# Optimization experiments

Hardware: AMD Instinct MI355X
Metric: run time of the kernel (lower is better)

The kernel has to match this reference:

```python
import jax, jax.numpy as jnp
import numpy as np

B, N, H, L, K, R = 1024, 64, 128, 4, 16, 20
CUTOFF = 5.0
GAMMA = 10.0   # RBF width
N_TYPES = 10

def _rn(k, shape, scale):
    return jax.random.normal(k, shape, jnp.float32) * scale

def setup_inputs():
    key = jax.random.key(0)
    ks = jax.random.split(key, 16)
    z = lambda *s: jnp.zeros(s, jnp.float32)
    return {
        "positions": _rn(ks[0], (B, N, 3), 2.0),
        "atomic_numbers": jax.random.randint(ks[1], (B, N), 0, N_TYPES),
        "atom_embed": _rn(ks[2], (N_TYPES, H // 4), 0.1),
        "pos_W": _rn(ks[3], (3, 3 * H // 4), 0.5),
        "pos_b": z(3 * H // 4),
        "msg_W": _rn(ks[4], (L, 2 * H + R, H), (2 * H + R) ** -0.5),
        "msg_b": z(L, H),
        "upd_W": _rn(ks[5], (L, H, H), H ** -0.5),
        "upd_b": z(L, H),
        "gself_W": _rn(ks[6], (L, H, H), H ** -0.5),
        "gmean_W": _rn(ks[7], (L, H, H), H ** -0.5),
        "g_b": z(L, H),
        "fus_W": _rn(ks[8], (L, 2 * H, H), (2 * H) ** -0.5),
        "fus_b": z(L, H),
        "ln_g": jnp.ones((L, H), jnp.float32),
        "ln_b": z(L, H),
        "cb_W1": _rn(ks[9], (L, H, 4 * H), H ** -0.5),
        "cb_b1": z(L, 4 * H),
        "cb_W2": _rn(ks[10], (L, 4 * H, H), (4 * H) ** -0.5),
        "cb_b2": z(L, H),
        "fo_W1": _rn(ks[11], (H, H), H ** -0.5),
        "fo_b1": z(H),
        "fo_W2": _rn(ks[12], (H, 3), H ** -0.5),
        "fo_b2": z(3),
    }

def _ln(x, g, b):
    m = x.mean(-1, keepdims=True)
    v = ((x - m) ** 2).mean(-1, keepdims=True)
    return (x - m) * jax.lax.rsqrt(v + 1e-5) * g + b

def reference(positions, atomic_numbers, atom_embed, pos_W, pos_b, msg_W, msg_b,
              upd_W, upd_b, gself_W, gmean_W, g_b, fus_W, fus_b, ln_g, ln_b,
              cb_W1, cb_b1, cb_W2, cb_b2, fo_W1, fo_b1, fo_W2, fo_b2):
    silu = jax.nn.silu
    Bb, Nn, _ = positions.shape
    # embeddings: atom type (H/4) || position (3H/4)
    h = jnp.concatenate([atom_embed[atomic_numbers], positions @ pos_W + pos_b], -1)  # [B,N,H]
    # kNN graph from positions (static across layers since positions are fixed)
    diff = positions[:, :, None, :] - positions[:, None, :, :]
    d2 = jnp.sum(diff * diff, -1) + jnp.eye(Nn, dtype=positions.dtype) * 1e9  # exclude self
    neg_d2, idx = jax.lax.top_k(-d2, K)                       # [B,N,K]
    d = jnp.sqrt(jnp.maximum(-neg_d2, 1e-12))
    centers = jnp.linspace(0.0, CUTOFF, R).astype(positions.dtype)
    rbf = jnp.exp(-GAMMA * (d[..., None] - centers) ** 2)     # [B,N,K,R]
    env = (0.5 * (jnp.cos(jnp.pi * d / CUTOFF) + 1.0) * (d < CUTOFF))[..., None]  # cosine cutoff
    idx_flat = idx.reshape(Bb, Nn * K)
    for i in range(msg_W.shape[0]):
        # local MPNN: gather neighbors, message MLP on [h_i, h_j, rbf], envelope, sum
        h_j = jnp.take_along_axis(h, idx_flat[:, :, None], axis=1).reshape(Bb, Nn, K, -1)
        h_i = jnp.broadcast_to(h[:, :, None, :], h_j.shape)
        m = silu(jnp.concatenate([h_i, h_j, rbf], -1) @ msg_W[i] + msg_b[i]) * env
        local = h + silu(m.sum(2) @ upd_W[i] + upd_b[i])
        # Clifford mean-field: self transform + global-mean transform
        glob = silu(h @ gself_W[i] + h.mean(1, keepdims=True) @ gmean_W[i] + g_b[i])
        # fusion (dropout is identity at inference)
        fused = silu(jnp.concatenate([local, glob], -1) @ fus_W[i] + fus_b[i])
        # Clifford block: pre-LN residual MLP
        x = _ln(fused, ln_g[i], ln_b[i])
        h = fused + silu(x @ cb_W1[i] + cb_b1[i]) @ cb_W2[i] + cb_b2[i]
    return silu(h @ fo_W1 + fo_b1) @ fo_W2 + fo_b2  # [B,N,3] forces
```

## Files before the change

kernel.cpp:

```cpp
#include <hip/hip_runtime.h>

typedef unsigned short ushort_t;
typedef unsigned int uint_t;
typedef unsigned long long ull_t;
typedef __attribute__((ext_vector_type(8))) short short8;
typedef __attribute__((ext_vector_type(4))) float f32x4;

#define B_ 1024
#define N_ 64
#define H_ 128
#define NT 256

#define IMG_WI 0
#define IMG_WJ 16384
#define IMG_UW 32768
#define IMG_GS 49152
#define IMG_FT 65536
#define IMG_FB 81920
#define IMG_C1 98304
#define IMG_C2 163840
#define IMG_GMT 229376
#define IMG_RW 245760
#define IMG_L 249856
#define IMG_FO 999424
#define WS_WEIGHTS (2u*1024u*1024u)
#define KNN_STRIDE 12288u

__device__ __forceinline__ ushort_t f2bf(float f) {
    uint_t u = __float_as_uint(f);
    return (ushort_t)((u + 0x7fffu + ((u >> 16) & 1u)) >> 16);
}
__device__ __forceinline__ float bf2f(ushort_t u) {
    union { uint_t i; float f; } v; v.i = ((uint_t)u) << 16; return v.f;
}
__device__ __forceinline__ float siluf(float x) { return x / (1.0f + __expf(-x)); }

__device__ __forceinline__ int sidx(int m, int k) {
    return m * H_ + (((k >> 3) ^ (m & 7)) << 3) + (k & 7);
}
__device__ __forceinline__ int fragoff(int m, int ch) {
    return m * H_ + ((ch ^ (m & 7)) << 3);
}

extern "C" __global__ __launch_bounds__(256)
void convert_weights(const float* __restrict__ msg_W, const float* __restrict__ upd_W,
                     const float* __restrict__ gself_W, const float* __restrict__ fus_W,
                     const float* __restrict__ cb_W1, const float* __restrict__ cb_W2,
                     const float* __restrict__ gmean_W, const float* __restrict__ fo_W1,
                     ushort_t* __restrict__ wimg)
{
    const int g = blockIdx.x;
    if (g >= 244) {
        int st = g - 244;
        ushort_t* dst = wimg + IMG_FO + st * 4096;
        for (int e = 0; e < 16; ++e) {
            int q = threadIdx.x * 16 + e;
            int n = q >> 7, k = q & 127;
            dst[q] = f2bf(fo_W1[(size_t)k * 128 + st * 32 + n]);
        }
        return;
    }
    const int l = g / 61, r = g - l * 61;
    ushort_t* base = wimg + l * IMG_L;
    if (r == 60) {
        const float* W = msg_W + l * 35328 + 256 * 128;
        ushort_t* dst = base + IMG_RW;
        for (int e = 0; e < 16; ++e) {
            int q = threadIdx.x * 16 + e;
            int sub = q >> 10, n = (q >> 5) & 31, k = q & 31;
            dst[q] = f2bf(k < 20 ? W[(size_t)k * 128 + sub * 32 + n] : 0.0f);
        }
        return;
    }
    const float* W; int ld = 128, k0 = 0, c0, off, st;
    if      (r < 4)  { W = msg_W + l * 35328;            st = r;      off = IMG_WI;  c0 = st * 32; }
    else if (r < 8)  { W = msg_W + l * 35328;  k0 = 128; st = r - 4;  off = IMG_WJ;  c0 = st * 32; }
    else if (r < 12) { W = upd_W + l * 16384;            st = r - 8;  off = IMG_UW;  c0 = st * 32; }
    else if (r < 16) { W = gself_W + l * 16384;          st = r - 12; off = IMG_GS;  c0 = st * 32; }
    else if (r < 20) { W = fus_W + l * 32768;            st = r - 16; off = IMG_FT;  c0 = st * 32; }
    else if (r < 24) { W = fus_W + l * 32768;  k0 = 128; st = r - 20; off = IMG_FB;  c0 = st * 32; }
    else if (r < 40) { W = cb_W1 + l * 65536;  ld = 512; st = r - 24; off = IMG_C1;  c0 = st * 32; }
    else if (r < 56) { int j = (r - 40) >> 2; W = cb_W2 + l * 65536; k0 = j * 128;
                       st = r - 40; off = IMG_C2; c0 = ((r - 40) & 3) * 32; }
    else             { W = gmean_W + l * 16384;          st = r - 56; off = IMG_GMT; c0 = st * 32; }
    ushort_t* dst = base + off + st * 4096;
    for (int e = 0; e < 16; ++e) {
        int q = threadIdx.x * 16 + e;
        int n = q >> 7, k = q & 127;
        dst[q] = f2bf(W[(size_t)(k0 + k) * ld + c0 + n]);
    }
}

extern "C" __global__ __launch_bounds__(64)
void knn_kernel(const float* __restrict__ positions, char* __restrict__ ws)
{
    const int b = blockIdx.x, lane = threadIdx.x;
    float px = positions[b * 192 + lane * 3 + 0];
    float py = positions[b * 192 + lane * 3 + 1];
    float pz = positions[b * 192 + lane * 3 + 2];
    float* kd = (float*)(ws + WS_WEIGHTS + (size_t)b * KNN_STRIDE);
    float* ke = kd + 1024;
    ushort_t* ki = (ushort_t*)(ke + 1024);
    for (int n = 0; n < 64; ++n) {
        float dx = __fsub_rn(__shfl(px, n), px);
        float dy = __fsub_rn(__shfl(py, n), py);
        float dz = __fsub_rn(__shfl(pz, n), pz);
        float d2 = __fadd_rn(__fadd_rn(__fmul_rn(dx, dx), __fmul_rn(dy, dy)), __fmul_rn(dz, dz));
        if (lane == n) d2 = 1e30f;
        float sd = 0.f; int si = 0;
        for (int k = 0; k < 16; ++k) {
            float dmin = d2;
            #pragma unroll
            for (int o = 1; o < 64; o <<= 1) dmin = fminf(dmin, __shfl_xor(dmin, o));
            ull_t mask = __ballot(d2 == dmin);
            int widx = __ffsll(mask) - 1;
            if (lane == widx) d2 = 1e30f;
            if (lane == k) { si = widx; sd = dmin; }
        }
        if (lane < 16) {
            float dd = sqrtf(fmaxf(sd, 1e-12f));
            kd[n * 16 + lane] = dd;
            ke[n * 16 + lane] = (dd < 5.0f) ? 0.5f * (__cosf(0.62831853071795864769f * dd) + 1.0f) : 0.0f;
            ki[n * 16 + lane] = (ushort_t)si;
        }
    }
}

struct __align__(16) Smem {
    ushort_t T1[N_ * H_];
    ushort_t T2[N_ * H_];
    ushort_t T3[N_ * H_];
    float d[1024];
    float env[1024];
    ushort_t idx[1024];
    char u[2048];
};

__device__ __forceinline__ f32x4 gemm_s(const short8 a[4], const ushort_t* __restrict__ img,
                                        int s, int l15, int quad)
{
    const ushort_t* base = img + ((s >> 1) << 12) + ((((s & 1) << 4) + l15) << 7) + quad * 8;
    short8 b0 = *(const short8*)(base);
    short8 b1 = *(const short8*)(base + 32);
    short8 b2 = *(const short8*)(base + 64);
    short8 b3 = *(const short8*)(base + 96);
    f32x4 c = {0.f, 0.f, 0.f, 0.f};
    c = __builtin_amdgcn_mfma_f32_16x16x32_bf16(a[0], b0, c, 0, 0, 0);
    c = __builtin_amdgcn_mfma_f32_16x16x32_bf16(a[1], b1, c, 0, 0, 0);
    c = __builtin_amdgcn_mfma_f32_16x16x32_bf16(a[2], b2, c, 0, 0, 0);
    c = __builtin_amdgcn_mfma_f32_16x16x32_bf16(a[3], b3, c, 0, 0, 0);
    return c;
}
__device__ __forceinline__ f32x4 gemm_s_acc(const short8 a[4], const ushort_t* __restrict__ img,
                                            int s, int l15, int quad, f32x4 c)
{
    const ushort_t* base = img + ((s >> 1) << 12) + ((((s & 1) << 4) + l15) << 7) + quad * 8;
    short8 b0 = *(const short8*)(base);
    short8 b1 = *(const short8*)(base + 32);
    short8 b2 = *(const short8*)(base + 64);
    short8 b3 = *(const short8*)(base + 96);
    c = __builtin_amdgcn_mfma_f32_16x16x32_bf16(a[0], b0, c, 0, 0, 0);
    c = __builtin_amdgcn_mfma_f32_16x16x32_bf16(a[1], b1, c, 0, 0, 0);
    c = __builtin_amdgcn_mfma_f32_16x16x32_bf16(a[2], b2, c, 0, 0, 0);
    c = __builtin_amdgcn_mfma_f32_16x16x32_bf16(a[3], b3, c, 0, 0, 0);
    return c;
}
__device__ __forceinline__ void loadA(const ushort_t* __restrict__ X, int mrow, int quad, short8 a[4]) {
    #pragma unroll
    for (int kc = 0; kc < 4; ++kc) a[kc] = *(const short8*)&X[fragoff(mrow, kc * 4 + quad)];
}

extern "C" __global__ __launch_bounds__(NT, 2)
void md17_fused_kernel(
    const float* __restrict__ positions, const int* __restrict__ atomic_numbers,
    const float* __restrict__ atom_embed, const float* __restrict__ pos_W,
    const float* __restrict__ pos_b,
    const float* __restrict__ msg_b, const float* __restrict__ upd_b,
    const float* __restrict__ g_b, const float* __restrict__ fus_b,
    const float* __restrict__ ln_g, const float* __restrict__ ln_b,
    const float* __restrict__ cb_b1, const float* __restrict__ cb_b2,
    const float* __restrict__ fo_b1,
    const float* __restrict__ fo_W2, const float* __restrict__ fo_b2,
    char* __restrict__ ws, float* __restrict__ out)
{
    __shared__ Smem sm;
    const int b = blockIdx.x;
    const int tid = threadIdx.x;
    const int wave = tid >> 6, lane = tid & 63;
    const int quad = lane >> 4, l15 = lane & 15;
    const int mrow = wave * 16 + l15;
    const int rbase = wave * 16 + quad * 4;

    const ushort_t* wimg = (const ushort_t*)ws;
    float* spos = (float*)sm.u;
    ushort_t* part = (ushort_t*)sm.u;
    float* hmean = (float*)(sm.u + 1024);
    float* gvec  = (float*)(sm.u + 1536);

    float hreg[8][4];

    {
        const char* kb = ws + WS_WEIGHTS + (size_t)b * KNN_STRIDE;
        const float* kd = (const float*)kb;
        const float* ke = (const float*)(kb + 4096);
        const uint_t* ki = (const uint_t*)(kb + 8192);
        for (int t = tid; t < 1024; t += NT) { sm.d[t] = kd[t]; sm.env[t] = ke[t]; }
        for (int t = tid; t < 512; t += NT) ((uint_t*)sm.idx)[t] = ki[t];
        if (tid < 192) spos[tid] = positions[b * 192 + tid];
    }
    __syncthreads();
    {
        int an[4];
        #pragma unroll
        for (int r = 0; r < 4; ++r) an[r] = atomic_numbers[b * N_ + rbase + r];
        #pragma unroll
        for (int s = 0; s < 8; ++s) {
            int col = s * 16 + l15;
            #pragma unroll
            for (int r = 0; r < 4; ++r) {
                float v;
                if (s < 2) {
                    v = atom_embed[an[r] * 32 + col];
                } else {
                    int j = col - 32;
                    v = pos_b[j];
                    #pragma unroll
                    for (int c = 0; c < 3; ++c)
                        v = fmaf(spos[(rbase + r) * 3 + c], pos_W[c * 96 + j], v);
                }
                hreg[s][r] = v;
                sm.T3[sidx(rbase + r, col)] = f2bf(v);
            }
        }
    }
    __syncthreads();

    #pragma unroll 1
    for (int l = 0; l < 4; ++l) {
        const ushort_t* wl = wimg + l * IMG_L;
        const float* mb  = msg_b + l * H_;
        const float* ub  = upd_b + l * H_;
        const float* gb  = g_b + l * H_;
        const float* fb  = fus_b + l * H_;
        const float* lg  = ln_g + l * H_;
        const float* lb  = ln_b + l * H_;
        const float* c1b = cb_b1 + l * 4 * H_;
        const float* c2b = cb_b2 + l * H_;

        #pragma unroll
        for (int s = 0; s < 8; ++s) {
            int col = s * 16 + l15;
            float p = hreg[s][0] + hreg[s][1] + hreg[s][2] + hreg[s][3];
            p += __shfl_xor(p, 16);
            p += __shfl_xor(p, 32);
            if (quad == 0) part[wave * 128 + col] = f2bf(p);
        }
        __syncthreads();
        if (tid < H_)
            hmean[tid] = (bf2f(part[tid]) + bf2f(part[128 + tid])
                        + bf2f(part[256 + tid]) + bf2f(part[384 + tid])) * (1.0f / 64.0f);
        __syncthreads();

        if (tid < H_) {
            float s = gb[tid];
            const ushort_t* wrow = wl + IMG_GMT + tid * 128;
            for (int c = 0; c < 128; c += 8) {
                short8 w = *(const short8*)(wrow + c);
                #pragma unroll
                for (int i = 0; i < 8; ++i) s = fmaf(hmean[c + i], bf2f((ushort_t)w[i]), s);
            }
            gvec[tid] = s;
        }
        {
            short8 a_h[4]; loadA(sm.T3, mrow, quad, a_h);
            #pragma unroll
            for (int s = 0; s < 8; ++s) {
                f32x4 c = gemm_s(a_h, wl + IMG_WI, s, l15, quad);
                int col = s * 16 + l15; float bv = mb[col];
                #pragma unroll
                for (int r = 0; r < 4; ++r)
                    sm.T1[sidx(rbase + r, col)] = f2bf(c[r] + bv);
            }
            #pragma unroll
            for (int s = 0; s < 8; ++s) {
                f32x4 c = gemm_s(a_h, wl + IMG_WJ, s, l15, quad);
                int col = s * 16 + l15;
                #pragma unroll
                for (int r = 0; r < 4; ++r)
                    sm.T2[sidx(rbase + r, col)] = f2bf(c[r]);
            }
        }
        __syncthreads();

        {
            float ccv[8];
            #pragma unroll
            for (int j = 0; j < 8; ++j)
                ccv[j] = (float)((double)(quad * 8 + j) * (5.0 / 19.0));
            #pragma unroll 1
            for (int g = 0; g < 16; ++g) {
                int n = wave * 16 + g;
                int jv[4]; float ev[4];
                #pragma unroll
                for (int r = 0; r < 4; ++r) {
                    int k = quad * 4 + r;
                    jv[r] = sm.idx[n * 16 + k];
                    ev[r] = sm.env[n * 16 + k];
                }
                float ddm = sm.d[n * 16 + l15];
                short8 arb;
                #pragma unroll
                for (int j = 0; j < 8; ++j) {
                    float t2 = ddm - ccv[j];
                    float rv = __expf(-10.0f * t2 * t2);
                    arb[j] = (short)((quad * 8 + j) < 20 ? f2bf(rv) : (ushort_t)0);
                }
                #pragma unroll
                for (int s = 0; s < 8; ++s) {
                    int col = s * 16 + l15;
                    const ushort_t* rbase_p = wl + IMG_RW + ((s >> 1) << 10)
                                            + ((((s & 1) << 4) + l15) << 5) + quad * 8;
                    short8 brw = *(const short8*)rbase_p;
                    f32x4 c = {0.f, 0.f, 0.f, 0.f};
                    c = __builtin_amdgcn_mfma_f32_16x16x32_bf16(arb, brw, c, 0, 0, 0);
                    float ai = bf2f(sm.T1[sidx(n, col)]);
                    float acc = 0.f;
                    #pragma unroll
                    for (int r = 0; r < 4; ++r) {
                        float gm = bf2f(sm.T2[sidx(jv[r], col)]);
                        acc = fmaf(siluf(ai + gm + c[r]), ev[r], acc);
                    }
                    acc += __shfl_xor(acc, 16);
                    acc += __shfl_xor(acc, 32);
                    if (quad == 0) sm.T1[sidx(n, col)] = f2bf(acc);
                }
            }
        }
        __syncthreads();


        {
            short8 a_m[4]; loadA(sm.T1, mrow, quad, a_m);
            #pragma unroll
            for (int s = 0; s < 8; ++s) {
                f32x4 c = gemm_s(a_m, wl + IMG_UW, s, l15, quad);
                int col = s * 16 + l15; float bv = ub[col];
                #pragma unroll
                for (int r = 0; r < 4; ++r)
                    sm.T2[sidx(rbase + r, col)] = f2bf(hreg[s][r] + siluf(c[r] + bv));
            }
            short8 a_h[4]; loadA(sm.T3, mrow, quad, a_h);
            #pragma unroll
            for (int s = 0; s < 8; ++s) {
                f32x4 c = gemm_s(a_h, wl + IMG_GS, s, l15, quad);
                int col = s * 16 + l15; float gv = gvec[col];
                #pragma unroll
                for (int r = 0; r < 4; ++r)
                    sm.T1[sidx(rbase + r, col)] = f2bf(siluf(c[r] + gv));
            }
        }

        float sr[4] = {0.f, 0.f, 0.f, 0.f}, qr[4] = {0.f, 0.f, 0.f, 0.f};
        {
            short8 a_t[4];
            loadA(sm.T2, mrow, quad, a_t);
            #pragma unroll
            for (int s = 0; s < 8; ++s) {
                f32x4 c = gemm_s(a_t, wl + IMG_FT, s, l15, quad);
                #pragma unroll
                for (int r = 0; r < 4; ++r) hreg[s][r] = c[r];
            }
            loadA(sm.T1, mrow, quad, a_t);
            #pragma unroll
            for (int s = 0; s < 8; ++s) {
                f32x4 c = gemm_s(a_t, wl + IMG_FB, s, l15, quad);
                int col = s * 16 + l15; float bv = fb[col];
                #pragma unroll
                for (int r = 0; r < 4; ++r) {
                    float v = siluf(hreg[s][r] + c[r] + bv);
                    hreg[s][r] = v;
                    sr[r] += v; qr[r] += v * v;
                }
            }
            #pragma unroll
            for (int o = 1; o < 16; o <<= 1) {
                #pragma unroll
                for (int r = 0; r < 4; ++r) {
                    sr[r] += __shfl_xor(sr[r], o);
                    qr[r] += __shfl_xor(qr[r], o);
                }
            }
        }

        #pragma unroll
        for (int r = 0; r < 4; ++r) {
            float mu = sr[r] * (1.0f / 128.0f);
            float var = qr[r] * (1.0f / 128.0f) - mu * mu;
            float rs = rsqrtf(var + 1e-5f);
            int row = rbase + r;
            #pragma unroll
            for (int s = 0; s < 8; ++s) {
                int col = s * 16 + l15;
                sm.T1[sidx(row, col)] = f2bf((hreg[s][r] - mu) * rs * lg[col] + lb[col]);
            }
        }

        {
            f32x4 acc2[8];
            #pragma unroll
            for (int s = 0; s < 8; ++s) {
                int col = s * 16 + l15; float bv = c2b[col];
                #pragma unroll
                for (int r = 0; r < 4; ++r) acc2[s][r] = hreg[s][r] + bv;
            }
            #pragma unroll 1
            for (int j = 0; j < 4; ++j) {
                short8 a_x[4]; loadA(sm.T1, mrow, quad, a_x);
                #pragma unroll
                for (int s = 0; s < 8; ++s) {
                    f32x4 c = gemm_s(a_x, wl + IMG_C1 + j * 16384, s, l15, quad);
                    int col = s * 16 + l15; float bv = c1b[j * H_ + col];
                    #pragma unroll
                    for (int r = 0; r < 4; ++r)
                        sm.T2[sidx(rbase + r, col)] = f2bf(siluf(c[r] + bv));
                }
                short8 a_t[4]; loadA(sm.T2, mrow, quad, a_t);
                #pragma unroll
                for (int s = 0; s < 8; ++s)
                    acc2[s] = gemm_s_acc(a_t, wl + IMG_C2 + j * 16384, s, l15, quad, acc2[s]);
            }
            #pragma unroll
            for (int s = 0; s < 8; ++s) {
                #pragma unroll
                for (int r = 0; r < 4; ++r) {
                    float v = acc2[s][r];
                    hreg[s][r] = v;
                    sm.T3[sidx(rbase + r, s * 16 + l15)] = f2bf(v);
                }
            }
        }
    }

    {
        short8 a_f[4]; loadA(sm.T3, mrow, quad, a_f);
        #pragma unroll
        for (int s = 0; s < 8; ++s) {
            f32x4 c = gemm_s(a_f, wimg + IMG_FO, s, l15, quad);
            int col = s * 16 + l15; float bv = fo_b1[col];
            #pragma unroll
            for (int r = 0; r < 4; ++r)
                sm.T2[sidx(rbase + r, col)] = f2bf(siluf(c[r] + bv));
        }
    }
    __syncthreads();
    if (tid < 192) {
        int n = tid / 3, j = tid - n * 3;
        float s = fo_b2[j];
        #pragma unroll 1
        for (int ch = 0; ch < 16; ++ch) {
            short8 v = *(const short8*)&sm.T2[fragoff(n, ch)];
            #pragma unroll
            for (int i = 0; i < 8; ++i)
                s = fmaf(bf2f((ushort_t)v[i]), fo_W2[(ch * 8 + i) * 3 + j], s);
        }
        out[b * 192 + tid] = s;
    }
}

extern "C" void kernel_launch(void* const* d_in, const int* in_sizes, int n_in,
                              void* d_out, int out_size, void* d_ws, size_t ws_size,
                              hipStream_t stream) {
    (void)in_sizes; (void)n_in; (void)out_size; (void)ws_size;
    convert_weights<<<248, 256, 0, stream>>>(
        (const float*)d_in[5], (const float*)d_in[7], (const float*)d_in[9],
        (const float*)d_in[12], (const float*)d_in[16], (const float*)d_in[18],
        (const float*)d_in[10], (const float*)d_in[20], (ushort_t*)d_ws);
    knn_kernel<<<B_, 64, 0, stream>>>((const float*)d_in[0], (char*)d_ws);
    md17_fused_kernel<<<B_, NT, 0, stream>>>(
        (const float*)d_in[0], (const int*)d_in[1],
        (const float*)d_in[2], (const float*)d_in[3], (const float*)d_in[4],
        (const float*)d_in[6], (const float*)d_in[8],
        (const float*)d_in[11], (const float*)d_in[13],
        (const float*)d_in[14], (const float*)d_in[15],
        (const float*)d_in[17], (const float*)d_in[19],
        (const float*)d_in[21],
        (const float*)d_in[22], (const float*)d_in[23],
        (char*)d_ws, (float*)d_out);
}
```

Baseline: 1.434 ms.

## Fuse kNN into main kernel, tile weight conversion via LDS, hoist RBF weights

```diff
diff --git a/kernel.cpp b/kernel.cpp
--- a/kernel.cpp
+++ b/kernel.cpp
@@ -23,12 +23,9 @@
 #define IMG_RW 245760
 #define IMG_L 249856
 #define IMG_FO 999424
-#define WS_WEIGHTS (2u*1024u*1024u)
-#define KNN_STRIDE 12288u
 
 __device__ __forceinline__ ushort_t f2bf(float f) {
-    uint_t u = __float_as_uint(f);
-    return (ushort_t)((u + 0x7fffu + ((u >> 16) & 1u)) >> 16);
+    return __builtin_bit_cast(ushort_t, (__bf16)f);
 }
 __device__ __forceinline__ float bf2f(ushort_t u) {
     union { uint_t i; float f; } v; v.i = ((uint_t)u) << 16; return v.f;
@@ -49,80 +46,55 @@
                      const float* __restrict__ gmean_W, const float* __restrict__ fo_W1,
                      ushort_t* __restrict__ wimg)
 {
+    __shared__ ushort_t tile[128][34];
     const int g = blockIdx.x;
+    const int tid = threadIdx.x;
+    const float* W; int ld = 128, k0 = 0, c0; ushort_t* dst;
     if (g >= 244) {
         int st = g - 244;
-        ushort_t* dst = wimg + IMG_FO + st * 4096;
-        for (int e = 0; e < 16; ++e) {
-            int q = threadIdx.x * 16 + e;
-            int n = q >> 7, k = q & 127;
-            dst[q] = f2bf(fo_W1[(size_t)k * 128 + st * 32 + n]);
-        }
-        return;
-    }
-    const int l = g / 61, r = g - l * 61;
-    ushort_t* base = wimg + l * IMG_L;
-    if (r == 60) {
-        const float* W = msg_W + l * 35328 + 256 * 128;
-        ushort_t* dst = base + IMG_RW;
-        for (int e = 0; e < 16; ++e) {
-            int q = threadIdx.x * 16 + e;
-            int sub = q >> 10, n = (q >> 5) & 31, k = q & 31;
-            dst[q] = f2bf(k < 20 ? W[(size_t)k * 128 + sub * 32 + n] : 0.0f);
-        }
-        return;
-    }
-    const float* W; int ld = 128, k0 = 0, c0, off, st;
-    if      (r < 4)  { W = msg_W + l * 35328;            st = r;      off = IMG_WI;  c0 = st * 32; }
-    else if (r < 8)  { W = msg_W + l * 35328;  k0 = 128; st = r - 4;  off = IMG_WJ;  c0 = st * 32; }
-    else if (r < 12) { W = upd_W + l * 16384;            st = r - 8;  off = IMG_UW;  c0 = st * 32; }
-    else if (r < 16) { W = gself_W + l * 16384;          st = r - 12; off = IMG_GS;  c0 = st * 32; }
-    else if (r < 20) { W = fus_W + l * 32768;            st = r - 16; off = IMG_FT;  c0 = st * 32; }
-    else if (r < 24) { W = fus_W + l * 32768;  k0 = 128; st = r - 20; off = IMG_FB;  c0 = st * 32; }
-    else if (r < 40) { W = cb_W1 + l * 65536;  ld = 512; st = r - 24; off = IMG_C1;  c0 = st * 32; }
-    else if (r < 56) { int j = (r - 40) >> 2; W = cb_W2 + l * 65536; k0 = j * 128;
-                       st = r - 40; off = IMG_C2; c0 = ((r - 40) & 3) * 32; }
-    else             { W = gmean_W + l * 16384;          st = r - 56; off = IMG_GMT; c0 = st * 32; }
-    ushort_t* dst = base + off + st * 4096;
-    for (int e = 0; e < 16; ++e) {
-        int q = threadIdx.x * 16 + e;
-        int n = q >> 7, k = q & 127;
-        dst[q] = f2bf(W[(size_t)(k0 + k) * ld + c0 + n]);
-    }
-}
-
-extern "C" __global__ __launch_bounds__(64)
-void knn_kernel(const float* __restrict__ positions, char* __restrict__ ws)
-{
-    const int b = blockIdx.x, lane = threadIdx.x;
-    float px = positions[b * 192 + lane * 3 + 0];
-    float py = positions[b * 192 + lane * 3 + 1];
-    float pz = positions[b * 192 + lane * 3 + 2];
-    float* kd = (float*)(ws + WS_WEIGHTS + (size_t)b * KNN_STRIDE);
-    float* ke = kd + 1024;
-    ushort_t* ki = (ushort_t*)(ke + 1024);
-    for (int n = 0; n < 64; ++n) {
-        float dx = __fsub_rn(__shfl(px, n), px);
-        float dy = __fsub_rn(__shfl(py, n), py);
-        float dz = __fsub_rn(__shfl(pz, n), pz);
-        float d2 = __fadd_rn(__fadd_rn(__fmul_rn(dx, dx), __fmul_rn(dy, dy)), __fmul_rn(dz, dz));
-        if (lane == n) d2 = 1e30f;
-        float sd = 0.f; int si = 0;
-        for (int k = 0; k < 16; ++k) {
-            float dmin = d2;
-            #pragma unroll
-            for (int o = 1; o < 64; o <<= 1) dmin = fminf(dmin, __shfl_xor(dmin, o));
-            ull_t mask = __ballot(d2 == dmin);
-            int widx = __ffsll(mask) - 1;
-            if (lane == widx) d2 = 1e30f;
-            if (lane == k) { si = widx; sd = dmin; }
-        }
-        if (lane < 16) {
-            float dd = sqrtf(fmaxf(sd, 1e-12f));
-            kd[n * 16 + lane] = dd;
-            ke[n * 16 + lane] = (dd < 5.0f) ? 0.5f * (__cosf(0.62831853071795864769f * dd) + 1.0f) : 0.0f;
-            ki[n * 16 + lane] = (ushort_t)si;
-        }
+        W = fo_W1; c0 = st * 32; dst = wimg + IMG_FO + st * 4096;
+    } else {
+        const int l = g / 61, r = g - l * 61;
+        ushort_t* base = wimg + l * IMG_L;
+        if (r == 60) {
+            const float* Wr = msg_W + l * 35328 + 256 * 128;
+            ushort_t* drw = base + IMG_RW;
+            for (int e = 0; e < 16; ++e) {
+                int q = threadIdx.x * 16 + e;
+                int sub = q >> 10, n = (q >> 5) & 31, k = q & 31;
+                drw[q] = f2bf(k < 20 ? Wr[(size_t)k * 128 + sub * 32 + n] : 0.0f);
+            }
+            return;
+        }
+        int off, st;
+        if      (r < 4)  { W = msg_W + l * 35328;            st = r;      off = IMG_WI;  c0 = st * 32; }
+        else if (r < 8)  { W = msg_W + l * 35328;  k0 = 128; st = r - 4;  off = IMG_WJ;  c0 = st * 32; }
+        else if (r < 12) { W = upd_W + l * 16384;            st = r - 8;  off = IMG_UW;  c0 = st * 32; }
+        else if (r < 16) { W = gself_W + l * 16384;          st = r - 12; off = IMG_GS;  c0 = st * 32; }
+        else if (r < 20) { W = fus_W + l * 32768;            st = r - 16; off = IMG_FT;  c0 = st * 32; }
+        else if (r < 24) { W = fus_W + l * 32768;  k0 = 128; st = r - 20; off = IMG_FB;  c0 = st * 32; }
+        else if (r < 40) { W = cb_W1 + l * 65536;  ld = 512; st = r - 24; off = IMG_C1;  c0 = st * 32; }
+        else if (r < 56) { int j = (r - 40) >> 2; W = cb_W2 + l * 65536; k0 = j * 128;
+                           st = r - 40; off = IMG_C2; c0 = ((r - 40) & 3) * 32; }
+        else             { W = gmean_W + l * 16384;          st = r - 56; off = IMG_GMT; c0 = st * 32; }
+        dst = base + off + st * 4096;
+    }
+    const int kr = tid >> 5, n = tid & 31;
+    #pragma unroll
+    for (int p = 0; p < 16; ++p) {
+        int k = p * 8 + kr;
+        tile[k][n] = f2bf(W[(size_t)(k0 + k) * ld + c0 + n]);
+    }
+    __syncthreads();
+    {
+        int n2 = tid >> 3, kk = (tid & 7) << 4;
+        short8 v0, v1;
+        #pragma unroll
+        for (int e = 0; e < 8; ++e) v0[e] = (short)tile[kk + e][n2];
+        #pragma unroll
+        for (int e = 0; e < 8; ++e) v1[e] = (short)tile[kk + 8 + e][n2];
+        *(short8*)(dst + n2 * 128 + kk) = v0;
+        *(short8*)(dst + n2 * 128 + kk + 8) = v1;
     }
 }
 
@@ -200,13 +172,35 @@
     float hreg[8][4];
 
     {
-        const char* kb = ws + WS_WEIGHTS + (size_t)b * KNN_STRIDE;
-        const float* kd = (const float*)kb;
-        const float* ke = (const float*)(kb + 4096);
-        const uint_t* ki = (const uint_t*)(kb + 8192);
-        for (int t = tid; t < 1024; t += NT) { sm.d[t] = kd[t]; sm.env[t] = ke[t]; }
-        for (int t = tid; t < 512; t += NT) ((uint_t*)sm.idx)[t] = ki[t];
+        float px = positions[b * 192 + lane * 3 + 0];
+        float py = positions[b * 192 + lane * 3 + 1];
+        float pz = positions[b * 192 + lane * 3 + 2];
         if (tid < 192) spos[tid] = positions[b * 192 + tid];
+        #pragma unroll 1
+        for (int g = 0; g < 16; ++g) {
+            int n = wave * 16 + g;
+            float dx = __fsub_rn(__shfl(px, n), px);
+            float dy = __fsub_rn(__shfl(py, n), py);
+            float dz = __fsub_rn(__shfl(pz, n), pz);
+            float d2 = __fadd_rn(__fadd_rn(__fmul_rn(dx, dx), __fmul_rn(dy, dy)), __fmul_rn(dz, dz));
+            if (lane == n) d2 = 1e30f;
+            float sd = 0.f; int si = 0;
+            for (int k = 0; k < 16; ++k) {
+                float dmin = d2;
+                #pragma unroll
+                for (int o = 1; o < 64; o <<= 1) dmin = fminf(dmin, __shfl_xor(dmin, o));
+                ull_t mask = __ballot(d2 == dmin);
+                int widx = __ffsll(mask) - 1;
+                if (lane == widx) d2 = 1e30f;
+                if (lane == k) { si = widx; sd = dmin; }
+            }
+            if (lane < 16) {
+                float dd = sqrtf(fmaxf(sd, 1e-12f));
+                sm.d[n * 16 + lane] = dd;
+                sm.env[n * 16 + lane] = (dd < 5.0f) ? 0.5f * (__cosf(0.62831853071795864769f * dd) + 1.0f) : 0.0f;
+                sm.idx[n * 16 + lane] = (ushort_t)si;
+            }
+        }
     }
     __syncthreads();
     {
@@ -234,6 +228,14 @@
         }
     }
     __syncthreads();
+    #pragma unroll
+    for (int s = 0; s < 8; ++s) {
+        int col = s * 16 + l15;
+        float p = hreg[s][0] + hreg[s][1] + hreg[s][2] + hreg[s][3];
+        p += __shfl_xor(p, 16);
+        p += __shfl_xor(p, 32);
+        if (quad == 0) part[wave * 128 + col] = f2bf(p);
+    }
 
     #pragma unroll 1
     for (int l = 0; l < 4; ++l) {
@@ -247,14 +249,6 @@
         const float* c1b = cb_b1 + l * 4 * H_;
         const float* c2b = cb_b2 + l * H_;
 
-        #pragma unroll
-        for (int s = 0; s < 8; ++s) {
-            int col = s * 16 + l15;
-            float p = hreg[s][0] + hreg[s][1] + hreg[s][2] + hreg[s][3];
-            p += __shfl_xor(p, 16);
-            p += __shfl_xor(p, 32);
-            if (quad == 0) part[wave * 128 + col] = f2bf(p);
-        }
         __syncthreads();
         if (tid < H_)
             hmean[tid] = (bf2f(part[tid]) + bf2f(part[128 + tid])
@@ -297,6 +291,11 @@
             #pragma unroll
             for (int j = 0; j < 8; ++j)
                 ccv[j] = (float)((double)(quad * 8 + j) * (5.0 / 19.0));
+            short8 brw[8];
+            #pragma unroll
+            for (int s = 0; s < 8; ++s)
+                brw[s] = *(const short8*)(wl + IMG_RW + ((s >> 1) << 10)
+                                          + ((((s & 1) << 4) + l15) << 5) + quad * 8);
             #pragma unroll 1
             for (int g = 0; g < 16; ++g) {
                 int n = wave * 16 + g;
@@ -318,11 +317,8 @@
                 #pragma unroll
                 for (int s = 0; s < 8; ++s) {
                     int col = s * 16 + l15;
-                    const ushort_t* rbase_p = wl + IMG_RW + ((s >> 1) << 10)
-                                            + ((((s & 1) << 4) + l15) << 5) + quad * 8;
-                    short8 brw = *(const short8*)rbase_p;
                     f32x4 c = {0.f, 0.f, 0.f, 0.f};
-                    c = __builtin_amdgcn_mfma_f32_16x16x32_bf16(arb, brw, c, 0, 0, 0);
+                    c = __builtin_amdgcn_mfma_f32_16x16x32_bf16(arb, brw[s], c, 0, 0, 0);
                     float ai = bf2f(sm.T1[sidx(n, col)]);
                     float acc = 0.f;
                     #pragma unroll
@@ -431,12 +427,18 @@
             }
             #pragma unroll
             for (int s = 0; s < 8; ++s) {
+                int col = s * 16 + l15;
+                float p = 0.f;
                 #pragma unroll
                 for (int r = 0; r < 4; ++r) {
                     float v = acc2[s][r];
                     hreg[s][r] = v;
-                    sm.T3[sidx(rbase + r, s * 16 + l15)] = f2bf(v);
-                }
+                    sm.T3[sidx(rbase + r, col)] = f2bf(v);
+                    p += v;
+                }
+                p += __shfl_xor(p, 16);
+                p += __shfl_xor(p, 32);
+                if (quad == 0) part[wave * 128 + col] = f2bf(p);
             }
         }
     }
@@ -475,7 +477,6 @@
         (const float*)d_in[5], (const float*)d_in[7], (const float*)d_in[9],
         (const float*)d_in[12], (const float*)d_in[16], (const float*)d_in[18],
         (const float*)d_in[10], (const float*)d_in[20], (ushort_t*)d_ws);
-    knn_kernel<<<B_, 64, 0, stream>>>((const float*)d_in[0], (char*)d_ws);
     md17_fused_kernel<<<B_, NT, 0, stream>>>(
         (const float*)d_in[0], (const int*)d_in[1],
         (const float*)d_in[2], (const float*)d_in[3], (const float*)d_in[4],
```

Result: faster. 1.347 ms (-6.1%).
